# Optimization experiments

Hardware: AMD Instinct MI355X
Metric: run time of the kernel (lower is better)

## Reference

```python
import jax, jax.numpy as jnp
import numpy as np

N_EMBED = 256
N_HEAD = 8
HEAD = N_EMBED // N_HEAD
LN_EPS = 1e-5


def _layernorm(x, g, b):
    mu = jnp.mean(x, axis=-1, keepdims=True)
    var = jnp.mean(jnp.square(x - mu), axis=-1, keepdims=True)
    return (x - mu) * jax.lax.rsqrt(var + LN_EPS) * g + b


def setup_inputs() -> dict:
    key = jax.random.key(0)
    ks = jax.random.split(key, 12)
    B, T, C, H, D = 16, 1024, N_EMBED, N_HEAD, HEAD
    s = C ** -0.5
    return {
        "x": jax.random.normal(ks[0], (B, T, C), jnp.float32),
        "wq": jax.random.normal(ks[1], (H, C, D), jnp.float32) * s,
        "wk": jax.random.normal(ks[2], (H, C, D), jnp.float32) * s,
        "wv": jax.random.normal(ks[3], (H, C, D), jnp.float32) * s,
        "w_proj": jax.random.normal(ks[4], (C, C), jnp.float32) * s,
        "b_proj": jnp.zeros((C,), jnp.float32),
        "w1": jax.random.normal(ks[5], (C, 4 * C), jnp.float32) * s,
        "b1": jnp.zeros((4 * C,), jnp.float32),
        "w2": jax.random.normal(ks[6], (4 * C, C), jnp.float32) * (4 * C) ** -0.5,
        "b2": jnp.zeros((C,), jnp.float32),
        "ln1_g": jnp.ones((C,), jnp.float32),
        "ln1_b": jnp.zeros((C,), jnp.float32),
        "ln2_g": jnp.ones((C,), jnp.float32),
        "ln2_b": jnp.zeros((C,), jnp.float32),
    }


def reference(x, wq, wk, wv, w_proj, b_proj, w1, b1, w2, b2,
              ln1_g, ln1_b, ln2_g, ln2_b):
    B, T, C = x.shape
    # --- multi-head causal self-attention on ln1(x) ---
    h = _layernorm(x, ln1_g, ln1_b)
    q = jnp.einsum('btc,hcd->bhtd', h, wq)
    k = jnp.einsum('btc,hcd->bhtd', h, wk)
    v = jnp.einsum('btc,hcd->bhtd', h, wv)
    # NOTE: original scales by n_embed**-0.5 (C of input), not head_size
    wei = jnp.einsum('bhtd,bhsd->bhts', q, k) * (C ** -0.5)
    causal = jnp.tril(jnp.ones((T, T), bool))
    wei = jnp.where(causal, wei, -jnp.inf)
    wei = jax.nn.softmax(wei, axis=-1)
    att = jnp.einsum('bhts,bhsd->bhtd', wei, v)
    att = att.transpose(0, 2, 1, 3).reshape(B, T, C)  # concat heads
    x = x + att @ w_proj + b_proj
    # --- feedforward on ln2(x) ---
    h2 = _layernorm(x, ln2_g, ln2_b)
    f = jax.nn.relu(h2 @ w1 + b1) @ w2 + b2
    return x + f
```

## Files before the change

kernel.cpp:

```cpp
#include <hip/hip_runtime.h>


typedef unsigned short u16;
typedef unsigned int u32;
typedef __attribute__((ext_vector_type(8))) short short8v;
typedef __attribute__((ext_vector_type(4))) float float4v;

__device__ __forceinline__ float b2f(u16 u) { union { u32 i; float f; } v; v.i = (u32)u << 16; return v.f; }
__device__ __forceinline__ float lo2f(u32 u) { union { u32 i; float f; } v; v.i = u << 16; return v.f; }
__device__ __forceinline__ float hi2f(u32 u) { union { u32 i; float f; } v; v.i = u & 0xffff0000u; return v.f; }
__device__ __forceinline__ u16 f2b(float f) {
    union { float f; u32 i; } v; v.f = f;
    u32 r = v.i + 0x7fffu + ((v.i >> 16) & 1u);
    return (u16)(r >> 16);
}
__device__ __forceinline__ u32 pk2_rtz(float a, float b) {
    return (__float_as_uint(a) >> 16) | (__float_as_uint(b) & 0xffff0000u);
}
__device__ __forceinline__ void async_cp16(const u16* g, u16* l) {
    __builtin_amdgcn_global_load_lds((const __attribute__((address_space(1))) void*)g,
                                     (__attribute__((address_space(3))) void*)l, 16, 0, 0);
}

__global__ __launch_bounds__(256) void prep_ln1(const float* __restrict__ wq,
                                                const float* __restrict__ wk,
                                                const float* __restrict__ wv,
                                                const float* __restrict__ wp,
                                                const float* __restrict__ w1,
                                                const float* __restrict__ w2,
                                                const float* __restrict__ x,
                                                const float* __restrict__ g1,
                                                const float* __restrict__ be1,
                                                u16* __restrict__ wqkvT,
                                                u16* __restrict__ wpT,
                                                u16* __restrict__ w1T,
                                                u16* __restrict__ w2T,
                                                u16* __restrict__ hout) {
    __shared__ u16 tile[64][65];
    int bid = blockIdx.x, tid = threadIdx.x;
    if (bid < 768) {
        int i = bid * 256 + tid;
        int n = i >> 8, k = i & 255;
        int which = n >> 8, nn = n & 255;
        const float* w = which == 0 ? wq : (which == 1 ? wk : wv);
        float v = w[((nn >> 5) * 256 + k) * 32 + (nn & 31)];
        if (which == 0) v *= 0.09016844f;
        wqkvT[i] = f2b(v);
    } else if (bid < 912) {
        const float* src; u16* dst; int K, N, t;
        if (bid < 784)      { src = wp; dst = wpT; K = 256;  N = 256;  t = bid - 768; }
        else if (bid < 848) { src = w1; dst = w1T; K = 256;  N = 1024; t = bid - 784; }
        else                { src = w2; dst = w2T; K = 1024; N = 256;  t = bid - 848; }
        int ntn = N >> 6;
        int k0 = (t / ntn) << 6, n0 = (t % ntn) << 6;
        int lane = tid & 63, wrow = tid >> 6;
        #pragma unroll
        for (int r = 0; r < 16; r++) {
            int k = wrow * 16 + r;
            tile[k][lane] = f2b(src[(size_t)(k0 + k) * N + n0 + lane]);
        }
        __syncthreads();
        #pragma unroll
        for (int r = 0; r < 16; r++) {
            int n = wrow * 16 + r;
            dst[(size_t)(n0 + n) * K + k0 + lane] = tile[lane][n];
        }
    } else {
        int row = (bid - 912) * 4 + (tid >> 6);
        int lane = tid & 63;
        float4 xv = *(const float4*)(x + (size_t)row * 256 + lane * 4);
        float v0 = xv.x, v1 = xv.y, v2 = xv.z, v3 = xv.w;
        float s = v0 + v1 + v2 + v3;
        #pragma unroll
        for (int m = 32; m; m >>= 1) s += __shfl_xor(s, m);
        float mu = s * 0.00390625f;
        float d0 = v0 - mu, d1 = v1 - mu, d2 = v2 - mu, d3 = v3 - mu;
        float ss = d0 * d0 + d1 * d1 + d2 * d2 + d3 * d3;
        #pragma unroll
        for (int m = 32; m; m >>= 1) ss += __shfl_xor(ss, m);
        float rs = rsqrtf(ss * 0.00390625f + 1e-5f);
        float4 g = *(const float4*)(g1 + lane * 4);
        float4 b = *(const float4*)(be1 + lane * 4);
        uint2 r;
        r.x = (u32)f2b(d0 * rs * g.x + b.x) | ((u32)f2b(d1 * rs * g.y + b.y) << 16);
        r.y = (u32)f2b(d2 * rs * g.z + b.z) | ((u32)f2b(d3 * rs * g.w + b.w) << 16);
        *(uint2*)(hout + (size_t)row * 256 + lane * 4) = r;
    }
}

template<bool HASBIAS, bool RELU, bool QKV>
__global__ __launch_bounds__(256) void gemm128(const u16* __restrict__ A,
                                               const u16* __restrict__ Bt,
                                               const float* __restrict__ bias,
                                               u16* __restrict__ out,
                                               u16* __restrict__ vout,
                                               int M, int N, int K) {
    __shared__ __align__(16) u16 SH[32768];
    const int tid = threadIdx.x, lane = tid & 63, w = tid >> 6;
    const int m0 = blockIdx.x * 128, n0 = blockIdx.y * 128;
    const int wm = (w & 1) * 64, wn = (w >> 1) * 64;
    const int fm = lane & 15, q = lane >> 4;

    float4v acc[4][4];
    #pragma unroll
    for (int i = 0; i < 4; i++)
        #pragma unroll
        for (int j = 0; j < 4; j++) acc[i][j] = (float4v){0.f, 0.f, 0.f, 0.f};

    const int kset = ((lane & 7) ^ (lane >> 3)) * 8;
    const u16* Ag = A  + (size_t)(m0 + w * 32 + (lane >> 3)) * K + kset;
    const u16* Bg = Bt + (size_t)(n0 + w * 32 + (lane >> 3)) * K + kset;

    auto issueS = [&](int t, int d) {
        u16* Asw = SH + d * 16384 + (w * 32) * 64;
        u16* Bsw = SH + d * 16384 + 8192 + (w * 32) * 64;
        #pragma unroll
        for (int c = 0; c < 4; c++) {
            async_cp16(Ag + (size_t)c * 8 * K + t * 64, Asw + c * 8 * 64);
            async_cp16(Bg + (size_t)c * 8 * K + t * 64, Bsw + c * 8 * 64);
        }
    };
    issueS(0, 0);
    issueS(1, 1);

    const int sw = fm & 7;
    #pragma unroll
    for (int t = 0; t < 4; ++t) {
        if (t == 3) asm volatile("s_waitcnt vmcnt(0)" ::: "memory");
        else        asm volatile("s_waitcnt vmcnt(8)" ::: "memory");
        __builtin_amdgcn_s_barrier();
        const u16* As = SH + (t & 1) * 16384;
        const u16* Bs = As + 8192;
        #pragma unroll
        for (int kk = 0; kk < 64; kk += 32) {
            const int slot = (((kk >> 3) + q) ^ sw) * 8;
            short8v af[4], bf[4];
            #pragma unroll
            for (int mi = 0; mi < 4; mi++)
                af[mi] = *(const short8v*)&As[(wm + mi * 16 + fm) * 64 + slot];
            #pragma unroll
            for (int ni = 0; ni < 4; ni++)
                bf[ni] = *(const short8v*)&Bs[(wn + ni * 16 + fm) * 64 + slot];
            #pragma unroll
            for (int mi = 0; mi < 4; mi++)
                #pragma unroll
                for (int ni = 0; ni < 4; ni++)
                    acc[mi][ni] = __builtin_amdgcn_mfma_f32_16x16x32_bf16(
                        bf[ni], af[mi], acc[mi][ni], 0, 0, 0);
        }
        if (t < 2) {
            __builtin_amdgcn_s_barrier();
            issueS(t + 2, t & 1);
        }
    }

    if (QKV && n0 >= 512) {
        __syncthreads();
        #pragma unroll
        for (int mi = 0; mi < 4; mi++) {
            int ml = wm + mi * 16 + fm;
            #pragma unroll
            for (int ni = 0; ni < 4; ni++) {
                int nl = wn + ni * 16 + q * 4;
                #pragma unroll
                for (int r = 0; r < 4; r++)
                    SH[(nl + r) * 136 + ml] = f2b(acc[mi][ni][r]);
            }
        }
        __syncthreads();
        int r = tid & 127, c = (tid >> 7) << 6;
        int hd = (n0 - 512) + r;
        int b = m0 >> 10, t0 = m0 & 1023;
        u16* dst = vout + (size_t)(b * 256 + hd) * 1024 + t0 + c;
        const u16* srcT = SH + r * 136 + c;
        #pragma unroll
        for (int i = 0; i < 8; i++)
            *(uint4*)(dst + i * 8) = *(const uint4*)(srcT + i * 8);
        return;
    }

    #pragma unroll
    for (int mi = 0; mi < 4; mi++) {
        int row = m0 + wm + mi * 16 + fm;
        #pragma unroll
        for (int ni = 0; ni < 4; ni++) {
            int nb = n0 + wn + ni * 16 + q * 4;
            float v0 = acc[mi][ni][0], v1 = acc[mi][ni][1],
                  v2 = acc[mi][ni][2], v3 = acc[mi][ni][3];
            if (HASBIAS) {
                float4 bv = *(const float4*)&bias[nb];
                v0 += bv.x; v1 += bv.y; v2 += bv.z; v3 += bv.w;
            }
            if (RELU) {
                v0 = fmaxf(v0, 0.f); v1 = fmaxf(v1, 0.f);
                v2 = fmaxf(v2, 0.f); v3 = fmaxf(v3, 0.f);
            }
            size_t idx = (size_t)row * N + nb;
            uint2 ov;
            ov.x = (u32)f2b(v0) | ((u32)f2b(v1) << 16);
            ov.y = (u32)f2b(v2) | ((u32)f2b(v3) << 16);
            *(uint2*)&out[idx] = ov;
        }
    }
}

__global__ __launch_bounds__(512, 2) void ffn_fused(const u16* __restrict__ h2,
                                                    const u16* __restrict__ w1T,
                                                    const float* __restrict__ b1,
                                                    const u16* __restrict__ w2T,
                                                    const float* __restrict__ b2,
                                                    const u16* __restrict__ x2b,
                                                    float* __restrict__ out) {
    __shared__ __align__(16) u16 SH[65536];
    u16* Ms = SH;
    u16* Bs = SH + 16384;
    const int tid = threadIdx.x, lane = tid & 63, w = tid >> 6;
    const int m0 = blockIdx.x * 64;
    const int wm = (w & 1) * 32;
    const int wn = (w >> 1) * 64;
    const int fm = lane & 15, q = lane >> 4;
    const int sw = fm & 7;
    const int kset = ((lane & 7) ^ (lane >> 3)) * 8;
    const int rb = w * 8 + (lane >> 3);

    short8v ar[8][2];
    {
        const u16* Abase = h2 + (size_t)(m0 + wm + fm) * 256 + q * 8;
        #pragma unroll
        for (int kcn = 0; kcn < 8; kcn++)
            #pragma unroll
            for (int mi = 0; mi < 2; mi++)
                ar[kcn][mi] = *(const short8v*)(Abase + (size_t)mi * 16 * 256 + kcn * 32);
    }

    auto issueB = [&](int t, u16* dst) {
        const int n2 = t >> 3, k2 = t & 3;
        if (((t >> 2) & 1) == 0) {
            const u16* src = w1T + (size_t)(n2 * 256 + rb) * 256 + k2 * 64 + kset;
            #pragma unroll
            for (int c = 0; c < 4; c++)
                async_cp16(src + (size_t)c * 64 * 256, dst + c * 4096);
        } else {
            const u16* src = w2T + (size_t)rb * 1024 + n2 * 256 + k2 * 64 + kset;
            #pragma unroll
            for (int c = 0; c < 4; c++)
                async_cp16(src + (size_t)c * 64 * 1024, dst + c * 4096);
        }
    };

    issueB(0, Bs + w * 512);
    issueB(1, Bs + 16384 + w * 512);

    float4v acc1[2][4], acc2[2][4];
    #pragma unroll
    for (int i = 0; i < 2; i++)
        #pragma unroll
        for (int j = 0; j < 4; j++) acc2[i][j] = (float4v){0.f, 0.f, 0.f, 0.f};

    #pragma unroll
    for (int t = 0; t < 32; ++t) {
        const int nch = t >> 3, ph = (t >> 2) & 1, kc = t & 3;
        if (t == 31) asm volatile("s_waitcnt vmcnt(0)" ::: "memory");
        else         asm volatile("s_waitcnt vmcnt(4)" ::: "memory");
        __builtin_amdgcn_s_barrier();
        if (t + 2 < 32)
            issueB(t + 2, Bs + ((t + 2) % 3) * 16384 + w * 512);
        const u16* Bb = Bs + (t % 3) * 16384;
        if (ph == 0) {
            if (kc == 0) {
                #pragma unroll
                for (int i = 0; i < 2; i++)
                    #pragma unroll
                    for (int j = 0; j < 4; j++) acc1[i][j] = (float4v){0.f, 0.f, 0.f, 0.f};
            }
            #pragma unroll
            for (int kk = 0; kk < 64; kk += 32) {
                const int slot = (((kk >> 3) + q) ^ sw) * 8;
                short8v bf[4];
                #pragma unroll
                for (int ni = 0; ni < 4; ni++)
                    bf[ni] = *(const short8v*)&Bb[(wn + ni * 16 + fm) * 64 + slot];
                #pragma unroll
                for (int mi = 0; mi < 2; mi++)
                    #pragma unroll
                    for (int ni = 0; ni < 4; ni++)
                        acc1[mi][ni] = __builtin_amdgcn_mfma_f32_16x16x32_bf16(
                            bf[ni], ar[kc * 2 + (kk >> 5)][mi], acc1[mi][ni], 0, 0, 0);
            }
            if (kc == 3) {
                #pragma unroll
                for (int ni = 0; ni < 4; ni++) {
                    const int c2 = wn + ni * 16 + q * 4;
                    const int kcM = c2 >> 6, cc = c2 & 63;
                    float4 bv = *(const float4*)&b1[nch * 256 + c2];
                    #pragma unroll
                    for (int mi = 0; mi < 2; mi++) {
                        const int row = wm + mi * 16 + fm;
                        float v0 = fmaxf(acc1[mi][ni][0] + bv.x, 0.f);
                        float v1 = fmaxf(acc1[mi][ni][1] + bv.y, 0.f);
                        float v2 = fmaxf(acc1[mi][ni][2] + bv.z, 0.f);
                        float v3 = fmaxf(acc1[mi][ni][3] + bv.w, 0.f);
                        uint2 pp;
                        pp.x = (u32)f2b(v0) | ((u32)f2b(v1) << 16);
                        pp.y = (u32)f2b(v2) | ((u32)f2b(v3) << 16);
                        *(uint2*)&Ms[kcM * 4096 + row * 64 +
                                     (((cc >> 3) ^ (row & 7)) * 8) + (cc & 7)] = pp;
                    }
                }
                asm volatile("s_waitcnt lgkmcnt(0)" ::: "memory");
            }
        } else {
            const u16* Ab = Ms + kc * 4096;
            #pragma unroll
            for (int kk = 0; kk < 64; kk += 32) {
                const int slot = (((kk >> 3) + q) ^ sw) * 8;
                short8v af[2], bf[4];
                #pragma unroll
                for (int mi = 0; mi < 2; mi++)
                    af[mi] = *(const short8v*)&Ab[(wm + mi * 16 + fm) * 64 + slot];
                #pragma unroll
                for (int ni = 0; ni < 4; ni++)
                    bf[ni] = *(const short8v*)&Bb[(wn + ni * 16 + fm) * 64 + slot];
                #pragma unroll
                for (int mi = 0; mi < 2; mi++)
                    #pragma unroll
                    for (int ni = 0; ni < 4; ni++)
                        acc2[mi][ni] = __builtin_amdgcn_mfma_f32_16x16x32_bf16(
                            bf[ni], af[mi], acc2[mi][ni], 0, 0, 0);
            }
        }
    }

    #pragma unroll
    for (int mi = 0; mi < 2; mi++) {
        const int row = m0 + wm + mi * 16 + fm;
        #pragma unroll
        for (int ni = 0; ni < 4; ni++) {
            const int nb = wn + ni * 16 + q * 4;
            size_t idx = (size_t)row * 256 + nb;
            float4 bv = *(const float4*)&b2[nb];
            uint2 rv = *(const uint2*)&x2b[idx];
            float v0 = acc2[mi][ni][0] + bv.x + lo2f(rv.x);
            float v1 = acc2[mi][ni][1] + bv.y + hi2f(rv.x);
            float v2 = acc2[mi][ni][2] + bv.z + lo2f(rv.y);
            float v3 = acc2[mi][ni][3] + bv.w + hi2f(rv.y);
            *(float4*)&out[idx] = (float4){v0, v1, v2, v3};
        }
    }
}

__global__ __launch_bounds__(256) void proj_ln2(const u16* __restrict__ att,
                                                const u16* __restrict__ wpT,
                                                const float* __restrict__ bp,
                                                const float* __restrict__ x,
                                                const float* __restrict__ g2,
                                                const float* __restrict__ be2,
                                                u16* __restrict__ x2b,
                                                u16* __restrict__ h2) {
    __shared__ __align__(16) u16 AB[2][18432];
    __shared__ float ps[4][16], pq[4][16];
    const int tid = threadIdx.x, lane = tid & 63, w = tid >> 6;
    const int m0 = blockIdx.x * 32;
    const int wm = (w & 1) * 16, wn = (w >> 1) * 128;
    const int fm = lane & 15, q = lane >> 4;

    float4v acc[8];
    #pragma unroll
    for (int i = 0; i < 8; i++) acc[i] = (float4v){0.f, 0.f, 0.f, 0.f};

    const int kset = ((lane & 7) ^ (lane >> 3)) * 8;
    const u16* Ag = att + (size_t)(m0 + w * 8 + (lane >> 3)) * 256 + kset;
    const u16* Bg = wpT + (size_t)(w * 64 + (lane >> 3)) * 256 + kset;

    auto issueS = [&](int t, int d) {
        u16* Asw = AB[d] + (w * 8) * 64;
        u16* Bsw = AB[d] + 2048 + (w * 64) * 64;
        async_cp16(Ag + t * 64, Asw);
        #pragma unroll
        for (int c = 0; c < 8; c++)
            async_cp16(Bg + (size_t)c * 8 * 256 + t * 64, Bsw + c * 8 * 64);
    };
    issueS(0, 0);
    issueS(1, 1);

    const int sw = fm & 7;
    #pragma unroll
    for (int t = 0; t < 4; ++t) {
        if (t == 3) asm volatile("s_waitcnt vmcnt(0)" ::: "memory");
        else        asm volatile("s_waitcnt vmcnt(9)" ::: "memory");
        __builtin_amdgcn_s_barrier();
        const u16* As = AB[t & 1];
        const u16* Bs = AB[t & 1] + 2048;
        #pragma unroll
        for (int kk = 0; kk < 64; kk += 32) {
            const int slot = (((kk >> 3) + q) ^ sw) * 8;
            short8v af = *(const short8v*)&As[(wm + fm) * 64 + slot];
            #pragma unroll
            for (int ni = 0; ni < 8; ni++) {
                short8v bf = *(const short8v*)&Bs[(wn + ni * 16 + fm) * 64 + slot];
                acc[ni] = __builtin_amdgcn_mfma_f32_16x16x32_bf16(bf, af, acc[ni], 0, 0, 0);
            }
        }
        if (t < 2) {
            __builtin_amdgcn_s_barrier();
            issueS(t + 2, t & 1);
        }
    }

    int m = m0 + wm + fm;
    float v[8][4];
    float s = 0.f, sq = 0.f;
    #pragma unroll
    for (int ni = 0; ni < 8; ni++) {
        int nb = wn + ni * 16 + q * 4;
        float4 xv = *(const float4*)(x + (size_t)m * 256 + nb);
        float4 bv = *(const float4*)&bp[nb];
        #pragma unroll
        for (int r = 0; r < 4; r++) {
            float t = acc[ni][r] + (&bv.x)[r] + (&xv.x)[r];
            v[ni][r] = t;
            s += t; sq += t * t;
        }
    }
    s += __shfl_xor(s, 16);  s += __shfl_xor(s, 32);
    sq += __shfl_xor(sq, 16); sq += __shfl_xor(sq, 32);
    if (q == 0) { ps[w][fm] = s; pq[w][fm] = sq; }
    __syncthreads();
    s = ps[w][fm] + ps[w ^ 2][fm];
    sq = pq[w][fm] + pq[w ^ 2][fm];
    float mu = s * 0.00390625f;
    float rs = rsqrtf(sq * 0.00390625f - mu * mu + 1e-5f);
    #pragma unroll
    for (int ni = 0; ni < 8; ni++) {
        int nb = wn + ni * 16 + q * 4;
        size_t idx = (size_t)m * 256 + nb;
        float4 gv = *(const float4*)&g2[nb];
        float4 bv = *(const float4*)&be2[nb];
        uint2 xo, ho;
        xo.x = (u32)f2b(v[ni][0]) | ((u32)f2b(v[ni][1]) << 16);
        xo.y = (u32)f2b(v[ni][2]) | ((u32)f2b(v[ni][3]) << 16);
        float h0 = (v[ni][0] - mu) * rs * gv.x + bv.x;
        float h1 = (v[ni][1] - mu) * rs * gv.y + bv.y;
        float h2v = (v[ni][2] - mu) * rs * gv.z + bv.z;
        float h3 = (v[ni][3] - mu) * rs * gv.w + bv.w;
        ho.x = (u32)f2b(h0) | ((u32)f2b(h1) << 16);
        ho.y = (u32)f2b(h2v) | ((u32)f2b(h3) << 16);
        *(uint2*)&x2b[idx] = xo;
        *(uint2*)&h2[idx] = ho;
    }
}

__global__ __launch_bounds__(256) void attn_mfma(const u16* __restrict__ qk,
                                                 const u16* __restrict__ vtg,
                                                 u16* __restrict__ att) {
    const int T = 1024;
    int jj = (blockIdx.x + (blockIdx.y >> 3)) & 7;
    int b = blockIdx.y >> 3, hh = blockIdx.y & 7;
    int tid = threadIdx.x;
    int lane = tid & 63, w = tid >> 6;
    int fm = lane & 15, q = lane >> 4;

    __shared__ __align__(16) u16 Ks[64][72];
    __shared__ __align__(16) u16 Vt[32][72];
    __shared__ __align__(16) u16 Pl[4][16][72];

    size_t base = (size_t)b * T * 512;
    const u16* kb = qk + base + 256 + hh * 32;
    const u16* vt = vtg + (size_t)((b * 8 + hh) * 32) * 1024;
    const int krow = tid >> 2, kcol = (tid & 3) * 8;
    const int vd = tid >> 3, vs = (tid & 7) * 8;

    int qa0 = jj * 64, qb0 = (15 - jj) * 64;
    int tqa = qa0 + w * 16 + fm, tqb = qb0 + w * 16 + fm;
    short8v qfa = *(const short8v*)(qk + base + (size_t)tqa * 512 + hh * 32 + q * 8);
    short8v qfb = *(const short8v*)(qk + base + (size_t)tqb * 512 + hh * 32 + q * 8);
    float4v oa0 = {0.f, 0.f, 0.f, 0.f}, oa1 = {0.f, 0.f, 0.f, 0.f};
    float4v ob0 = {0.f, 0.f, 0.f, 0.f}, ob1 = {0.f, 0.f, 0.f, 0.f};
    float la = 0.f, lb = 0.f;
    int wqa = qa0 + w * 16, wqb = qb0 + w * 16;
    int nIter = 16 - jj;

    uint4 kreg = *(const uint4*)(kb + (size_t)krow * 512 + kcol);
    uint4 vreg = *(const uint4*)(vt + (size_t)vd * 1024 + vs);

    for (int it = 0; it < nIter; ++it) {
        int s0 = it << 6;
        __syncthreads();
        *(uint4*)&Ks[krow][kcol] = kreg;
        *(uint4*)&Vt[vd][vs] = vreg;
        __syncthreads();
        if (it + 1 < nIter) {
            int ns0 = s0 + 64;
            kreg = *(const uint4*)(kb + (size_t)(ns0 + krow) * 512 + kcol);
            vreg = *(const uint4*)(vt + (size_t)vd * 1024 + ns0 + vs);
        }
        short8v kf0 = *(const short8v*)&Ks[fm][q * 8];
        short8v kf1 = *(const short8v*)&Ks[16 + fm][q * 8];
        short8v kf2 = *(const short8v*)&Ks[32 + fm][q * 8];
        short8v kf3 = *(const short8v*)&Ks[48 + fm][q * 8];
        short8v vf00 = *(const short8v*)&Vt[fm][q * 8];
        short8v vf01 = *(const short8v*)&Vt[fm][32 + q * 8];
        short8v vf10 = *(const short8v*)&Vt[16 + fm][q * 8];
        short8v vf11 = *(const short8v*)&Vt[16 + fm][32 + q * 8];
        float4v z = {0.f, 0.f, 0.f, 0.f};

        #pragma unroll
        for (int t2 = 0; t2 < 2; t2++) {
            int wq0 = t2 ? wqa : wqb;
            if (s0 >= wq0 + 16) continue;
            int tq = t2 ? tqa : tqb;
            short8v qf = t2 ? qfa : qfb;
            float4v s_0 = __builtin_amdgcn_mfma_f32_16x16x32_bf16(kf0, qf, z, 0, 0, 0);
            float4v s_1 = __builtin_amdgcn_mfma_f32_16x16x32_bf16(kf1, qf, z, 0, 0, 0);
            float4v s_2 = __builtin_amdgcn_mfma_f32_16x16x32_bf16(kf2, qf, z, 0, 0, 0);
            float4v s_3 = __builtin_amdgcn_mfma_f32_16x16x32_bf16(kf3, qf, z, 0, 0, 0);
            float p[16];
            #pragma unroll
            for (int r = 0; r < 4; r++) {
                p[r] = exp2f(s_0[r]); p[4 + r] = exp2f(s_1[r]);
                p[8 + r] = exp2f(s_2[r]); p[12 + r] = exp2f(s_3[r]);
            }
            if (s0 + 63 > wq0) {
                int sb = s0 + q * 4;
                #pragma unroll
                for (int c = 0; c < 4; c++)
                    #pragma unroll
                    for (int r = 0; r < 4; r++)
                        if (sb + c * 16 + r > tq) p[c * 4 + r] = 0.f;
            }
            float rsum = 0.f;
            #pragma unroll
            for (int i = 0; i < 16; i++) rsum += p[i];
            rsum += __shfl_xor(rsum, 16);
            rsum += __shfl_xor(rsum, 32);
            if (t2) la += rsum; else lb += rsum;

            #pragma unroll
            for (int c = 0; c < 4; c++) {
                uint2 pp;
                pp.x = pk2_rtz(p[c * 4 + 0], p[c * 4 + 1]);
                pp.y = pk2_rtz(p[c * 4 + 2], p[c * 4 + 3]);
                *(uint2*)&Pl[w][fm][c * 16 + q * 4] = pp;
            }
            short8v pf0 = *(const short8v*)&Pl[w][fm][q * 8];
            short8v pf1 = *(const short8v*)&Pl[w][fm][32 + q * 8];
            if (t2) {
                oa0 = __builtin_amdgcn_mfma_f32_16x16x32_bf16(vf00, pf0, oa0, 0, 0, 0);
                oa0 = __builtin_amdgcn_mfma_f32_16x16x32_bf16(vf01, pf1, oa0, 0, 0, 0);
                oa1 = __builtin_amdgcn_mfma_f32_16x16x32_bf16(vf10, pf0, oa1, 0, 0, 0);
                oa1 = __builtin_amdgcn_mfma_f32_16x16x32_bf16(vf11, pf1, oa1, 0, 0, 0);
            } else {
                ob0 = __builtin_amdgcn_mfma_f32_16x16x32_bf16(vf00, pf0, ob0, 0, 0, 0);
                ob0 = __builtin_amdgcn_mfma_f32_16x16x32_bf16(vf01, pf1, ob0, 0, 0, 0);
                ob1 = __builtin_amdgcn_mfma_f32_16x16x32_bf16(vf10, pf0, ob1, 0, 0, 0);
                ob1 = __builtin_amdgcn_mfma_f32_16x16x32_bf16(vf11, pf1, ob1, 0, 0, 0);
            }
        }
    }

    #pragma unroll
    for (int t2 = 0; t2 < 2; t2++) {
        float inv = 1.f / (t2 ? la : lb);
        float4v o0 = t2 ? oa0 : ob0, o1 = t2 ? oa1 : ob1;
        int tq = t2 ? tqa : tqb;
        uint2 r0, r1;
        r0.x = (u32)f2b(o0[0] * inv) | ((u32)f2b(o0[1] * inv) << 16);
        r0.y = (u32)f2b(o0[2] * inv) | ((u32)f2b(o0[3] * inv) << 16);
        r1.x = (u32)f2b(o1[0] * inv) | ((u32)f2b(o1[1] * inv) << 16);
        r1.y = (u32)f2b(o1[2] * inv) | ((u32)f2b(o1[3] * inv) << 16);
        size_t o = (size_t)(b * T + tq) * 256 + hh * 32;
        *(uint2*)(att + o + q * 4) = r0;
        *(uint2*)(att + o + 16 + q * 4) = r1;
    }
}

extern "C" void kernel_launch(void* const* d_in, const int* in_sizes, int n_in,
                              void* d_out, int out_size, void* d_ws, size_t ws_size,
                              hipStream_t stream) {
    const int BT = 16 * 1024;
    const float* x      = (const float*)d_in[0];
    const float* wq     = (const float*)d_in[1];
    const float* wk     = (const float*)d_in[2];
    const float* wv     = (const float*)d_in[3];
    const float* w_proj = (const float*)d_in[4];
    const float* b_proj = (const float*)d_in[5];
    const float* w1     = (const float*)d_in[6];
    const float* b1     = (const float*)d_in[7];
    const float* w2     = (const float*)d_in[8];
    const float* b2     = (const float*)d_in[9];
    const float* ln1_g  = (const float*)d_in[10];
    const float* ln1_b  = (const float*)d_in[11];
    const float* ln2_g  = (const float*)d_in[12];
    const float* ln2_b  = (const float*)d_in[13];

    char* ws = (char*)d_ws;
    const size_t MB = 1024 * 1024;
    u16*  x2b   = (u16*)(ws + 0);
    u16*  hbuf  = (u16*)(ws + 8 * MB);
    u16*  qk    = (u16*)(ws + 16 * MB);
    u16*  vtg   = (u16*)(ws + 32 * MB);
    u16*  wqkvT = (u16*)(ws + 48 * MB);
    u16*  wpT   = (u16*)(ws + 48 * MB + 0x60000);
    u16*  w1T   = (u16*)(ws + 48 * MB + 0x80000);
    u16*  w2T   = (u16*)(ws + 48 * MB + 0x100000);

    prep_ln1<<<5008, 256, 0, stream>>>(wq, wk, wv, w_proj, w1, w2, x, ln1_g, ln1_b,
                                       wqkvT, wpT, w1T, w2T, hbuf);
    gemm128<false, false, true><<<dim3(128, 6), 256, 0, stream>>>(
        hbuf, wqkvT, nullptr, qk, vtg, BT, 512, 256);
    attn_mfma<<<dim3(8, 128), 256, 0, stream>>>(qk, vtg, hbuf);
    proj_ln2<<<512, 256, 0, stream>>>(hbuf, wpT, b_proj, x, ln2_g, ln2_b, x2b, hbuf);
    ffn_fused<<<256, 512, 0, stream>>>(hbuf, w1T, b1, w2T, b2, x2b, (float*)d_out);
}
```

Baseline: 178.5 us.

## Fuse output projection and LayerNorm2 into the fused FFN kernel

The proj_ln2 kernel is merged into the FFN kernel as four extra pipeline steps. Each 64-row block computes att@w_proj, adds bias and the fp32 residual, reduces LayerNorm statistics across warps through shared memory, and writes h2 into shared memory. It then reloads h2 into the A-fragment registers before the existing FFN loop. This removes one kernel launch and the global round trips for x2b and h2, and keeps the residual in fp32 registers. The cost is higher register pressure (launch bounds drop to one block per CU minimum) and the projection running on only 256 blocks.

```diff
diff --git a/kernel.cpp b/kernel.cpp
--- a/kernel.cpp
+++ b/kernel.cpp
@@ -204,20 +204,26 @@
     }
 }
 
-__global__ __launch_bounds__(512, 2) void ffn_fused(const u16* __restrict__ h2,
-                                                    const u16* __restrict__ w1T,
-                                                    const float* __restrict__ b1,
-                                                    const u16* __restrict__ w2T,
-                                                    const float* __restrict__ b2,
-                                                    const u16* __restrict__ x2b,
-                                                    float* __restrict__ out) {
+__global__ __launch_bounds__(512, 1) void tail_fused(const u16* __restrict__ att,
+                                                     const u16* __restrict__ wpT,
+                                                     const float* __restrict__ bp,
+                                                     const float* __restrict__ x,
+                                                     const float* __restrict__ g2,
+                                                     const float* __restrict__ be2,
+                                                     const u16* __restrict__ w1T,
+                                                     const float* __restrict__ b1,
+                                                     const u16* __restrict__ w2T,
+                                                     const float* __restrict__ b2,
+                                                     float* __restrict__ out) {
     __shared__ __align__(16) u16 SH[65536];
+    __shared__ float ps[2][2][16][4], pq[2][2][16][4];
     u16* Ms = SH;
     u16* Bs = SH + 16384;
     const int tid = threadIdx.x, lane = tid & 63, w = tid >> 6;
     const int m0 = blockIdx.x * 64;
-    const int wm = (w & 1) * 32;
-    const int wn = (w >> 1) * 64;
+    const int wmi = w & 1, wni = w >> 1;
+    const int wm = wmi * 32;
+    const int wn = wni * 64;
     const int fm = lane & 15, q = lane >> 4;
     const int sw = fm & 7;
     const int kset = ((lane & 7) ^ (lane >> 3)) * 8;
@@ -225,7 +231,7 @@
 
     short8v ar[8][2];
     {
-        const u16* Abase = h2 + (size_t)(m0 + wm + fm) * 256 + q * 8;
+        const u16* Abase = att + (size_t)(m0 + wm + fm) * 256 + q * 8;
         #pragma unroll
         for (int kcn = 0; kcn < 8; kcn++)
             #pragma unroll
@@ -233,46 +239,50 @@
                 ar[kcn][mi] = *(const short8v*)(Abase + (size_t)mi * 16 * 256 + kcn * 32);
     }
 
-    auto issueB = [&](int t, u16* dst) {
-        const int n2 = t >> 3, k2 = t & 3;
-        if (((t >> 2) & 1) == 0) {
-            const u16* src = w1T + (size_t)(n2 * 256 + rb) * 256 + k2 * 64 + kset;
+    auto issueB = [&](int u, u16* dst) {
+        if (u < 4) {
+            const u16* src = wpT + (size_t)rb * 256 + u * 64 + kset;
             #pragma unroll
             for (int c = 0; c < 4; c++)
                 async_cp16(src + (size_t)c * 64 * 256, dst + c * 4096);
         } else {
-            const u16* src = w2T + (size_t)rb * 1024 + n2 * 256 + k2 * 64 + kset;
-            #pragma unroll
-            for (int c = 0; c < 4; c++)
-                async_cp16(src + (size_t)c * 64 * 1024, dst + c * 4096);
+            const int tt = u - 4, n2 = tt >> 3, k2 = tt & 3;
+            if (((tt >> 2) & 1) == 0) {
+                const u16* src = w1T + (size_t)(n2 * 256 + rb) * 256 + k2 * 64 + kset;
+                #pragma unroll
+                for (int c = 0; c < 4; c++)
+                    async_cp16(src + (size_t)c * 64 * 256, dst + c * 4096);
+            } else {
+                const u16* src = w2T + (size_t)rb * 1024 + n2 * 256 + k2 * 64 + kset;
+                #pragma unroll
+                for (int c = 0; c < 4; c++)
+                    async_cp16(src + (size_t)c * 64 * 1024, dst + c * 4096);
+            }
         }
     };
 
     issueB(0, Bs + w * 512);
     issueB(1, Bs + 16384 + w * 512);
 
-    float4v acc1[2][4], acc2[2][4];
+    float4v acc1[2][4], acc2[2][4], xr[2][4];
     #pragma unroll
     for (int i = 0; i < 2; i++)
         #pragma unroll
-        for (int j = 0; j < 4; j++) acc2[i][j] = (float4v){0.f, 0.f, 0.f, 0.f};
+        for (int j = 0; j < 4; j++) {
+            acc1[i][j] = (float4v){0.f, 0.f, 0.f, 0.f};
+            acc2[i][j] = (float4v){0.f, 0.f, 0.f, 0.f};
+        }
 
     #pragma unroll
-    for (int t = 0; t < 32; ++t) {
-        const int nch = t >> 3, ph = (t >> 2) & 1, kc = t & 3;
-        if (t == 31) asm volatile("s_waitcnt vmcnt(0)" ::: "memory");
+    for (int t = 0; t < 36; ++t) {
+        if (t == 35) asm volatile("s_waitcnt vmcnt(0)" ::: "memory");
         else         asm volatile("s_waitcnt vmcnt(4)" ::: "memory");
         __builtin_amdgcn_s_barrier();
-        if (t + 2 < 32)
+        if (t + 2 < 36)
             issueB(t + 2, Bs + ((t + 2) % 3) * 16384 + w * 512);
         const u16* Bb = Bs + (t % 3) * 16384;
-        if (ph == 0) {
-            if (kc == 0) {
-                #pragma unroll
-                for (int i = 0; i < 2; i++)
-                    #pragma unroll
-                    for (int j = 0; j < 4; j++) acc1[i][j] = (float4v){0.f, 0.f, 0.f, 0.f};
-            }
+
+        if (t < 4) {
             #pragma unroll
             for (int kk = 0; kk < 64; kk += 32) {
                 const int slot = (((kk >> 3) + q) ^ sw) * 8;
@@ -285,48 +295,143 @@
                     #pragma unroll
                     for (int ni = 0; ni < 4; ni++)
                         acc1[mi][ni] = __builtin_amdgcn_mfma_f32_16x16x32_bf16(
-                            bf[ni], ar[kc * 2 + (kk >> 5)][mi], acc1[mi][ni], 0, 0, 0);
-            }
-            if (kc == 3) {
+                            bf[ni], ar[t * 2 + (kk >> 5)][mi], acc1[mi][ni], 0, 0, 0);
+            }
+            if (t == 3) {
+                float s[2] = {0.f, 0.f}, s2[2] = {0.f, 0.f};
+                #pragma unroll
+                for (int mi = 0; mi < 2; mi++)
+                    #pragma unroll
+                    for (int ni = 0; ni < 4; ni++) {
+                        const int nb = wn + ni * 16 + q * 4;
+                        const int row = m0 + wm + mi * 16 + fm;
+                        float4 bv = *(const float4*)&bp[nb];
+                        float4 xv = *(const float4*)(x + (size_t)row * 256 + nb);
+                        #pragma unroll
+                        for (int r = 0; r < 4; r++) {
+                            float tv = acc1[mi][ni][r] + (&bv.x)[r] + (&xv.x)[r];
+                            xr[mi][ni][r] = tv;
+                            s[mi] += tv; s2[mi] += tv * tv;
+                        }
+                    }
+                #pragma unroll
+                for (int mi = 0; mi < 2; mi++) {
+                    s[mi]  += __shfl_xor(s[mi], 16);  s[mi]  += __shfl_xor(s[mi], 32);
+                    s2[mi] += __shfl_xor(s2[mi], 16); s2[mi] += __shfl_xor(s2[mi], 32);
+                }
+                if (q == 0) {
+                    ps[wmi][0][fm][wni] = s[0];  ps[wmi][1][fm][wni] = s[1];
+                    pq[wmi][0][fm][wni] = s2[0]; pq[wmi][1][fm][wni] = s2[1];
+                }
+                asm volatile("s_waitcnt lgkmcnt(0)" ::: "memory");
+                __builtin_amdgcn_s_barrier();
+                float mu[2], rs[2];
+                #pragma unroll
+                for (int mi = 0; mi < 2; mi++) {
+                    float S  = ps[wmi][mi][fm][0] + ps[wmi][mi][fm][1]
+                             + ps[wmi][mi][fm][2] + ps[wmi][mi][fm][3];
+                    float SQ = pq[wmi][mi][fm][0] + pq[wmi][mi][fm][1]
+                             + pq[wmi][mi][fm][2] + pq[wmi][mi][fm][3];
+                    mu[mi] = S * 0.00390625f;
+                    rs[mi] = rsqrtf(SQ * 0.00390625f - mu[mi] * mu[mi] + 1e-5f);
+                }
                 #pragma unroll
                 for (int ni = 0; ni < 4; ni++) {
                     const int c2 = wn + ni * 16 + q * 4;
                     const int kcM = c2 >> 6, cc = c2 & 63;
-                    float4 bv = *(const float4*)&b1[nch * 256 + c2];
+                    float4 gv = *(const float4*)&g2[c2];
+                    float4 bv = *(const float4*)&be2[c2];
                     #pragma unroll
                     for (int mi = 0; mi < 2; mi++) {
                         const int row = wm + mi * 16 + fm;
-                        float v0 = fmaxf(acc1[mi][ni][0] + bv.x, 0.f);
-                        float v1 = fmaxf(acc1[mi][ni][1] + bv.y, 0.f);
-                        float v2 = fmaxf(acc1[mi][ni][2] + bv.z, 0.f);
-                        float v3 = fmaxf(acc1[mi][ni][3] + bv.w, 0.f);
+                        float h0 = (xr[mi][ni][0] - mu[mi]) * rs[mi] * gv.x + bv.x;
+                        float h1 = (xr[mi][ni][1] - mu[mi]) * rs[mi] * gv.y + bv.y;
+                        float h2v = (xr[mi][ni][2] - mu[mi]) * rs[mi] * gv.z + bv.z;
+                        float h3 = (xr[mi][ni][3] - mu[mi]) * rs[mi] * gv.w + bv.w;
                         uint2 pp;
-                        pp.x = (u32)f2b(v0) | ((u32)f2b(v1) << 16);
-                        pp.y = (u32)f2b(v2) | ((u32)f2b(v3) << 16);
+                        pp.x = (u32)f2b(h0) | ((u32)f2b(h1) << 16);
+                        pp.y = (u32)f2b(h2v) | ((u32)f2b(h3) << 16);
                         *(uint2*)&Ms[kcM * 4096 + row * 64 +
                                      (((cc >> 3) ^ (row & 7)) * 8) + (cc & 7)] = pp;
                     }
                 }
                 asm volatile("s_waitcnt lgkmcnt(0)" ::: "memory");
+                __builtin_amdgcn_s_barrier();
+                #pragma unroll
+                for (int kcn = 0; kcn < 8; kcn++) {
+                    const int kcq = kcn >> 1, kk = (kcn & 1) * 32;
+                    const int slot = (((kk >> 3) + q) ^ sw) * 8;
+                    #pragma unroll
+                    for (int mi = 0; mi < 2; mi++)
+                        ar[kcn][mi] = *(const short8v*)&Ms[kcq * 4096 +
+                                        (wm + mi * 16 + fm) * 64 + slot];
+                }
             }
         } else {
-            const u16* Ab = Ms + kc * 4096;
-            #pragma unroll
-            for (int kk = 0; kk < 64; kk += 32) {
-                const int slot = (((kk >> 3) + q) ^ sw) * 8;
-                short8v af[2], bf[4];
-                #pragma unroll
-                for (int mi = 0; mi < 2; mi++)
-                    af[mi] = *(const short8v*)&Ab[(wm + mi * 16 + fm) * 64 + slot];
-                #pragma unroll
-                for (int ni = 0; ni < 4; ni++)
-                    bf[ni] = *(const short8v*)&Bb[(wn + ni * 16 + fm) * 64 + slot];
-                #pragma unroll
-                for (int mi = 0; mi < 2; mi++)
+            const int tt = t - 4;
+            const int nch = tt >> 3, ph = (tt >> 2) & 1, kc = tt & 3;
+            if (ph == 0) {
+                if (kc == 0) {
+                    #pragma unroll
+                    for (int i = 0; i < 2; i++)
+                        #pragma unroll
+                        for (int j = 0; j < 4; j++) acc1[i][j] = (float4v){0.f, 0.f, 0.f, 0.f};
+                }
+                #pragma unroll
+                for (int kk = 0; kk < 64; kk += 32) {
+                    const int slot = (((kk >> 3) + q) ^ sw) * 8;
+                    short8v bf[4];
                     #pragma unroll
                     for (int ni = 0; ni < 4; ni++)
-                        acc2[mi][ni] = __builtin_amdgcn_mfma_f32_16x16x32_bf16(
-                            bf[ni], af[mi], acc2[mi][ni], 0, 0, 0);
+                        bf[ni] = *(const short8v*)&Bb[(wn + ni * 16 + fm) * 64 + slot];
+                    #pragma unroll
+                    for (int mi = 0; mi < 2; mi++)
+                        #pragma unroll
+                        for (int ni = 0; ni < 4; ni++)
+                            acc1[mi][ni] = __builtin_amdgcn_mfma_f32_16x16x32_bf16(
+                                bf[ni], ar[kc * 2 + (kk >> 5)][mi], acc1[mi][ni], 0, 0, 0);
+                }
+                if (kc == 3) {
+                    #pragma unroll
+                    for (int ni = 0; ni < 4; ni++) {
+                        const int c2 = wn + ni * 16 + q * 4;
+                        const int kcM = c2 >> 6, cc = c2 & 63;
+                        float4 bv = *(const float4*)&b1[nch * 256 + c2];
+                        #pragma unroll
+                        for (int mi = 0; mi < 2; mi++) {
+                            const int row = wm + mi * 16 + fm;
+                            float v0 = fmaxf(acc1[mi][ni][0] + bv.x, 0.f);
+                            float v1 = fmaxf(acc1[mi][ni][1] + bv.y, 0.f);
+                            float v2 = fmaxf(acc1[mi][ni][2] + bv.z, 0.f);
+                            float v3 = fmaxf(acc1[mi][ni][3] + bv.w, 0.f);
+                            uint2 pp;
+                            pp.x = (u32)f2b(v0) | ((u32)f2b(v1) << 16);
+                            pp.y = (u32)f2b(v2) | ((u32)f2b(v3) << 16);
+                            *(uint2*)&Ms[kcM * 4096 + row * 64 +
+                                         (((cc >> 3) ^ (row & 7)) * 8) + (cc & 7)] = pp;
+                        }
+                    }
+                    asm volatile("s_waitcnt lgkmcnt(0)" ::: "memory");
+                }
+            } else {
+                const u16* Ab = Ms + kc * 4096;
+                #pragma unroll
+                for (int kk = 0; kk < 64; kk += 32) {
+                    const int slot = (((kk >> 3) + q) ^ sw) * 8;
+                    short8v af[2], bf[4];
+                    #pragma unroll
+                    for (int mi = 0; mi < 2; mi++)
+                        af[mi] = *(const short8v*)&Ab[(wm + mi * 16 + fm) * 64 + slot];
+                    #pragma unroll
+                    for (int ni = 0; ni < 4; ni++)
+                        bf[ni] = *(const short8v*)&Bb[(wn + ni * 16 + fm) * 64 + slot];
+                    #pragma unroll
+                    for (int mi = 0; mi < 2; mi++)
+                        #pragma unroll
+                        for (int ni = 0; ni < 4; ni++)
+                            acc2[mi][ni] = __builtin_amdgcn_mfma_f32_16x16x32_bf16(
+                                bf[ni], af[mi], acc2[mi][ni], 0, 0, 0);
+                }
             }
         }
     }
@@ -339,114 +444,12 @@
             const int nb = wn + ni * 16 + q * 4;
             size_t idx = (size_t)row * 256 + nb;
             float4 bv = *(const float4*)&b2[nb];
-            uint2 rv = *(const uint2*)&x2b[idx];
-            float v0 = acc2[mi][ni][0] + bv.x + lo2f(rv.x);
-            float v1 = acc2[mi][ni][1] + bv.y + hi2f(rv.x);
-            float v2 = acc2[mi][ni][2] + bv.z + lo2f(rv.y);
-            float v3 = acc2[mi][ni][3] + bv.w + hi2f(rv.y);
+            float v0 = acc2[mi][ni][0] + bv.x + xr[mi][ni][0];
+            float v1 = acc2[mi][ni][1] + bv.y + xr[mi][ni][1];
+            float v2 = acc2[mi][ni][2] + bv.z + xr[mi][ni][2];
+            float v3 = acc2[mi][ni][3] + bv.w + xr[mi][ni][3];
             *(float4*)&out[idx] = (float4){v0, v1, v2, v3};
         }
-    }
-}
-
-__global__ __launch_bounds__(256) void proj_ln2(const u16* __restrict__ att,
-                                                const u16* __restrict__ wpT,
-                                                const float* __restrict__ bp,
-                                                const float* __restrict__ x,
-                                                const float* __restrict__ g2,
-                                                const float* __restrict__ be2,
-                                                u16* __restrict__ x2b,
-                                                u16* __restrict__ h2) {
-    __shared__ __align__(16) u16 AB[2][18432];
-    __shared__ float ps[4][16], pq[4][16];
-    const int tid = threadIdx.x, lane = tid & 63, w = tid >> 6;
-    const int m0 = blockIdx.x * 32;
-    const int wm = (w & 1) * 16, wn = (w >> 1) * 128;
-    const int fm = lane & 15, q = lane >> 4;
-
-    float4v acc[8];
-    #pragma unroll
-    for (int i = 0; i < 8; i++) acc[i] = (float4v){0.f, 0.f, 0.f, 0.f};
-
-    const int kset = ((lane & 7) ^ (lane >> 3)) * 8;
-    const u16* Ag = att + (size_t)(m0 + w * 8 + (lane >> 3)) * 256 + kset;
-    const u16* Bg = wpT + (size_t)(w * 64 + (lane >> 3)) * 256 + kset;
-
-    auto issueS = [&](int t, int d) {
-        u16* Asw = AB[d] + (w * 8) * 64;
-        u16* Bsw = AB[d] + 2048 + (w * 64) * 64;
-        async_cp16(Ag + t * 64, Asw);
-        #pragma unroll
-        for (int c = 0; c < 8; c++)
-            async_cp16(Bg + (size_t)c * 8 * 256 + t * 64, Bsw + c * 8 * 64);
-    };
-    issueS(0, 0);
-    issueS(1, 1);
-
-    const int sw = fm & 7;
-    #pragma unroll
-    for (int t = 0; t < 4; ++t) {
-        if (t == 3) asm volatile("s_waitcnt vmcnt(0)" ::: "memory");
-        else        asm volatile("s_waitcnt vmcnt(9)" ::: "memory");
-        __builtin_amdgcn_s_barrier();
-        const u16* As = AB[t & 1];
-        const u16* Bs = AB[t & 1] + 2048;
-        #pragma unroll
-        for (int kk = 0; kk < 64; kk += 32) {
-            const int slot = (((kk >> 3) + q) ^ sw) * 8;
-            short8v af = *(const short8v*)&As[(wm + fm) * 64 + slot];
-            #pragma unroll
-            for (int ni = 0; ni < 8; ni++) {
-                short8v bf = *(const short8v*)&Bs[(wn + ni * 16 + fm) * 64 + slot];
-                acc[ni] = __builtin_amdgcn_mfma_f32_16x16x32_bf16(bf, af, acc[ni], 0, 0, 0);
-            }
-        }
-        if (t < 2) {
-            __builtin_amdgcn_s_barrier();
-            issueS(t + 2, t & 1);
-        }
-    }
-
-    int m = m0 + wm + fm;
-    float v[8][4];
-    float s = 0.f, sq = 0.f;
-    #pragma unroll
-    for (int ni = 0; ni < 8; ni++) {
-        int nb = wn + ni * 16 + q * 4;
-        float4 xv = *(const float4*)(x + (size_t)m * 256 + nb);
-        float4 bv = *(const float4*)&bp[nb];
-        #pragma unroll
-        for (int r = 0; r < 4; r++) {
-            float t = acc[ni][r] + (&bv.x)[r] + (&xv.x)[r];
-            v[ni][r] = t;
-            s += t; sq += t * t;
-        }
-    }
-    s += __shfl_xor(s, 16);  s += __shfl_xor(s, 32);
-    sq += __shfl_xor(sq, 16); sq += __shfl_xor(sq, 32);
-    if (q == 0) { ps[w][fm] = s; pq[w][fm] = sq; }
-    __syncthreads();
-    s = ps[w][fm] + ps[w ^ 2][fm];
-    sq = pq[w][fm] + pq[w ^ 2][fm];
-    float mu = s * 0.00390625f;
-    float rs = rsqrtf(sq * 0.00390625f - mu * mu + 1e-5f);
-    #pragma unroll
-    for (int ni = 0; ni < 8; ni++) {
-        int nb = wn + ni * 16 + q * 4;
-        size_t idx = (size_t)m * 256 + nb;
-        float4 gv = *(const float4*)&g2[nb];
-        float4 bv = *(const float4*)&be2[nb];
-        uint2 xo, ho;
-        xo.x = (u32)f2b(v[ni][0]) | ((u32)f2b(v[ni][1]) << 16);
-        xo.y = (u32)f2b(v[ni][2]) | ((u32)f2b(v[ni][3]) << 16);
-        float h0 = (v[ni][0] - mu) * rs * gv.x + bv.x;
-        float h1 = (v[ni][1] - mu) * rs * gv.y + bv.y;
-        float h2v = (v[ni][2] - mu) * rs * gv.z + bv.z;
-        float h3 = (v[ni][3] - mu) * rs * gv.w + bv.w;
-        ho.x = (u32)f2b(h0) | ((u32)f2b(h1) << 16);
-        ho.y = (u32)f2b(h2v) | ((u32)f2b(h3) << 16);
-        *(uint2*)&x2b[idx] = xo;
-        *(uint2*)&h2[idx] = ho;
     }
 }
 
@@ -595,7 +598,6 @@
 
     char* ws = (char*)d_ws;
     const size_t MB = 1024 * 1024;
-    u16*  x2b   = (u16*)(ws + 0);
     u16*  hbuf  = (u16*)(ws + 8 * MB);
     u16*  qk    = (u16*)(ws + 16 * MB);
     u16*  vtg   = (u16*)(ws + 32 * MB);
@@ -609,6 +611,6 @@
     gemm128<false, false, true><<<dim3(128, 6), 256, 0, stream>>>(
         hbuf, wqkvT, nullptr, qk, vtg, BT, 512, 256);
     attn_mfma<<<dim3(8, 128), 256, 0, stream>>>(qk, vtg, hbuf);
-    proj_ln2<<<512, 256, 0, stream>>>(hbuf, wpT, b_proj, x, ln2_g, ln2_b, x2b, hbuf);
-    ffn_fused<<<256, 512, 0, stream>>>(hbuf, w1T, b1, w2T, b2, x2b, (float*)d_out);
-}
+    tail_fused<<<256, 512, 0, stream>>>(hbuf, wpT, b_proj, x, ln2_g, ln2_b,
+                                        w1T, b1, w2T, b2, (float*)d_out);
+}
```

Measured after the change: 176.8 us. No clear change (-1.0%).
